# Optimization experiments

Hardware: AMD Instinct MI355X
Metric: run time of the kernel (lower is better)

## Reference

```python
import jax, jax.numpy as jnp
import numpy as np

C_, A_, B_ = 1, 128, 128          # image_size
H, Z, T, N = 512, 128, 16, 32     # h_dim, z_dim, steps, attention grid
EPS = 1e-8
BATCH = 256
PATCH = C_ * N * N                # read/write patch size (C_=1)
IN_ENC = 2 * PATCH + H


def gru_cell(x, h, W_ih, W_hh, b_ih, b_hh):
    gi = x @ W_ih.T + b_ih
    gh = h @ W_hh.T + b_hh
    i_r, i_z, i_n = jnp.split(gi, 3, axis=-1)
    h_r, h_z, h_n = jnp.split(gh, 3, axis=-1)
    r = jax.nn.sigmoid(i_r + h_r)
    z = jax.nn.sigmoid(i_z + h_z)
    n = jnp.tanh(i_n + r * h_n)
    return (1.0 - z) * n + z * h


def filterbank(gt, delta, two_sigma_sq, num_pixels):
    # gt, delta: [b,1]; two_sigma_sq: [b,1,1]
    g = 0.5 * (num_pixels + 1) * (gt + 1.0)                       # [b,1]
    grid = jnp.arange(N, dtype=jnp.float32) - 0.5 * (N - 1)       # [N]
    mu = g + grid[None, :] * delta                                # [b,N]
    pix = jnp.arange(num_pixels, dtype=jnp.float32)               # [P]
    F = jnp.exp(-(pix[None, None, :] - mu[:, :, None]) ** 2 / two_sigma_sq)
    return F / jnp.maximum(F.sum(axis=-1, keepdims=True), EPS)    # [b,N,P]


def get_filterbanks(h_dec, W_attn, b_attn):
    p = h_dec @ W_attn.T + b_attn                                 # [b,5]
    gt_x, gt_y, log_ss, log_dt, log_g = [p[:, i:i + 1] for i in range(5)]
    two_sigma_sq = (2.0 * jnp.exp(log_ss))[:, :, None]            # [b,1,1]
    delta = (max(A_, B_) - 1) * jnp.exp(log_dt) / (N - 1)         # [b,1]
    gamma = jnp.exp(log_g)                                        # [b,1]
    F_x = filterbank(gt_x, delta, two_sigma_sq, A_)               # [b,N,A]
    F_y = filterbank(gt_y, delta, two_sigma_sq, B_)               # [b,N,B]
    return F_x, F_y, gamma


def draw_forward(x, eps, W_ih_enc, W_hh_enc, b_ih_enc, b_hh_enc,
                 W_ih_dec, W_hh_dec, b_ih_dec, b_hh_dec,
                 W_mu, b_mu, W_ls, b_ls, W_wr, b_wr,
                 W_ra, b_ra, W_wa, b_wa):
    b = x.shape[0]
    xf = x.reshape(b, -1)                                         # [b, A*B]
    reconsts0 = jnp.zeros_like(xf)
    h0 = jnp.zeros((b, H), dtype=xf.dtype)

    def step(carry, eps_t):
        reconsts, h_enc, h_dec = carry
        # NOTE: faithful to original: reconsts[-1] is last batch row, broadcast
        x_hat = xf - jax.nn.sigmoid(reconsts[-1])
        # ---- read with attention ----
        F_x, F_y, gamma = get_filterbanks(h_dec, W_ra, b_ra)
        F_x_t = jnp.swapaxes(F_x, -1, -2)                         # [b,A,N]
        img = xf.reshape(b, A_, B_)
        img_hat = x_hat.reshape(b, A_, B_)
        x_attn = (F_y @ img @ F_x_t).reshape(b, -1)               # [b,N*N]
        xh_attn = (F_y @ img_hat @ F_x_t).reshape(b, -1)
        r = gamma * jnp.concatenate([x_attn, xh_attn], axis=1)    # [b,2*N*N]
        # ---- encoder GRU ----
        h_enc = gru_cell(jnp.concatenate([r, h_dec], axis=1), h_enc,
                         W_ih_enc, W_hh_enc, b_ih_enc, b_hh_enc)
        # ---- sample z ~ Q ----
        mu = h_enc @ W_mu.T + b_mu
        sigma = jnp.exp(h_enc @ W_ls.T + b_ls)
        z = mu + eps_t * sigma
        # ---- decoder GRU ----
        h_dec = gru_cell(z, h_dec, W_ih_dec, W_hh_dec, b_ih_dec, b_hh_dec)
        # ---- write with attention ----
        F_xw, F_yw, gamma_w = get_filterbanks(h_dec, W_wa, b_wa)
        w = (h_dec @ W_wr.T + b_wr).reshape(b, N, N)
        wr = (jnp.swapaxes(F_yw, -1, -2) @ w @ F_xw).reshape(b, -1) / gamma_w
        return (reconsts + wr, h_enc, h_dec), None

    (reconsts, _, _), _ = jax.lax.scan(step, (reconsts0, h0, h0), eps)
    return jax.nn.sigmoid(reconsts).reshape(-1, C_, A_, B_)


def setup_inputs() -> dict:
    key = jax.random.key(0)
    ks = jax.random.split(key, 24)
    s = 0.02
    inp = {
        "x": jax.random.uniform(ks[0], (BATCH, C_, A_, B_), jnp.float32),
        "eps": jax.random.normal(ks[1], (T, BATCH, Z), jnp.float32),
        "W_ih_enc": jax.random.normal(ks[2], (3 * H, IN_ENC), jnp.float32) * s,
        "W_hh_enc": jax.random.normal(ks[3], (3 * H, H), jnp.float32) * s,
        "b_ih_enc": jnp.zeros((3 * H,), jnp.float32),
        "b_hh_enc": jnp.zeros((3 * H,), jnp.float32),
        "W_ih_dec": jax.random.normal(ks[4], (3 * H, Z), jnp.float32) * s,
        "W_hh_dec": jax.random.normal(ks[5], (3 * H, H), jnp.float32) * s,
        "b_ih_dec": jnp.zeros((3 * H,), jnp.float32),
        "b_hh_dec": jnp.zeros((3 * H,), jnp.float32),
        "W_mu": jax.random.normal(ks[6], (Z, H), jnp.float32) * s,
        "b_mu": jnp.zeros((Z,), jnp.float32),
        "W_ls": jax.random.normal(ks[7], (Z, H), jnp.float32) * s,
        "b_ls": jnp.zeros((Z,), jnp.float32),
        "W_wr": jax.random.normal(ks[8], (PATCH, H), jnp.float32) * s,
        "b_wr": jnp.zeros((PATCH,), jnp.float32),
        "W_ra": jax.random.normal(ks[9], (5, H), jnp.float32) * s,
        "b_ra": jnp.zeros((5,), jnp.float32),
        "W_wa": jax.random.normal(ks[10], (5, H), jnp.float32) * s,
        "b_wa": jnp.zeros((5,), jnp.float32),
    }
    return inp


def reference(x, eps, W_ih_enc, W_hh_enc, b_ih_enc, b_hh_enc,
              W_ih_dec, W_hh_dec, b_ih_dec, b_hh_dec,
              W_mu, b_mu, W_ls, b_ls, W_wr, b_wr,
              W_ra, b_ra, W_wa, b_wa):
    return draw_forward(x, eps, W_ih_enc, W_hh_enc, b_ih_enc, b_hh_enc,
                        W_ih_dec, W_hh_dec, b_ih_dec, b_hh_dec,
                        W_mu, b_mu, W_ls, b_ls, W_wr, b_wr,
                        W_ra, b_ra, W_wa, b_wa)
```

## Files before the change

### kernel.cpp

```cpp
#include <hip/hip_runtime.h>
#include <math.h>

#define BATCHN 256
#define HDIM 512
#define ZDIM 128
#define NGRID 32
#define ABDIM 128
#define IMGSZ 16384
#define ENCIN 2560
#define G3 1536
#define SPLITK 4

typedef __attribute__((ext_vector_type(8))) short short8;
typedef __attribute__((ext_vector_type(4))) float f32x4;

__device__ __forceinline__ float sigmoidf_(float x){ return 1.0f/(1.0f+expf(-x)); }

__device__ __forceinline__ ushort f2bf_rne(float f){
    union{float f; uint u;} x; x.f=f;
    uint r = (x.u + 0x7FFFu + ((x.u>>16)&1u)) >> 16;
    return (ushort)r;
}
__device__ __forceinline__ float bf2f(ushort h){
    union{uint u; float f;} y; y.u = ((uint)h)<<16;
    return y.f;
}

__global__ void init_slast_k(float* __restrict__ s_last){
    int i = blockIdx.x*256 + threadIdx.x;
    s_last[i] = 0.5f;
}

__global__ void conv_w_k(const float* __restrict__ W, ushort* __restrict__ Wh,
                         ushort* __restrict__ Wl, int n4){
    int i = blockIdx.x*256 + threadIdx.x;
    if(i>=n4) return;
    float4 v = ((const float4*)W)[i];
    float f[4] = {v.x, v.y, v.z, v.w};
    ushort h[4], l[4];
    #pragma unroll
    for(int j=0;j<4;j++){
        h[j] = f2bf_rne(f[j]);
        l[j] = f2bf_rne(f[j] - bf2f(h[j]));
    }
    ushort4 hv; hv.x=h[0]; hv.y=h[1]; hv.z=h[2]; hv.w=h[3];
    ushort4 lv; lv.x=l[0]; lv.y=l[1]; lv.z=l[2]; lv.w=l[3];
    ((ushort4*)Wh)[i] = hv;
    ((ushort4*)Wl)[i] = lv;
}

__device__ __forceinline__ void attn_params_dev512(const float* __restrict__ h,
        const float* __restrict__ W, const float* __restrict__ bvec,
        float* red5 , float* pp , int tid){
    float accp[5];
    #pragma unroll
    for(int i=0;i<5;i++) accp[i]=0.f;
    for(int k=tid;k<HDIM;k+=512){
        float hv = h[k];
        #pragma unroll
        for(int i=0;i<5;i++) accp[i] += hv*W[i*HDIM+k];
    }
    int wv = tid>>6;
    #pragma unroll
    for(int i=0;i<5;i++){
        float a = accp[i];
        #pragma unroll
        for(int o=32;o>0;o>>=1) a += __shfl_down(a,o);
        if((tid&63)==0) red5[i*8+wv]=a;
    }
    __syncthreads();
    if(tid<5){
        float s = bvec[tid];
        #pragma unroll
        for(int w2=0;w2<8;w2++) s += red5[tid*8+w2];
        pp[tid]=s;
    }
    __syncthreads();
}

__device__ __forceinline__ void fill_fb_T(float* fxT, float* fyT, const float* pp, int tid){
    float gx = 64.5f*(pp[0]+1.0f);
    float gy = 64.5f*(pp[1]+1.0f);
    float tss = 2.0f*expf(pp[2]);
    float delta = (127.0f/31.0f)*expf(pp[3]);
    int rr = tid>>3;
    int q  = tid&7;
    int j  = rr&31;
    bool isY = rr>=32;
    float mu = (isY?gy:gx) + ((float)j-15.5f)*delta;
    float v[16]; float s=0.f;
    #pragma unroll
    for(int i=0;i<16;i++){
        float d = (float)(q*16+i)-mu;
        float e = expf(-d*d/tss);
        v[i]=e; s+=e;
    }
    s += __shfl_xor(s,1); s += __shfl_xor(s,2); s += __shfl_xor(s,4);
    float inv = 1.0f/fmaxf(s,1e-8f);
    float* dst = isY? fyT : fxT;
    #pragma unroll
    for(int i=0;i<16;i++) dst[(q*16+i)*32 + j] = v[i]*inv;
    __syncthreads();
}

__device__ __forceinline__ void fill_fb_R(float (*fx)[ABDIM+1], float (*fy)[ABDIM+1], const float* pp, int tid){
    float gx = 64.5f*(pp[0]+1.0f);
    float gy = 64.5f*(pp[1]+1.0f);
    float tss = 2.0f*expf(pp[2]);
    float delta = (127.0f/31.0f)*expf(pp[3]);
    int rr = tid>>3;
    int q  = tid&7;
    int j  = rr&31;
    bool isY = rr>=32;
    float mu = (isY?gy:gx) + ((float)j-15.5f)*delta;
    float v[16]; float s=0.f;
    #pragma unroll
    for(int i=0;i<16;i++){
        float d = (float)(q*16+i)-mu;
        float e = expf(-d*d/tss);
        v[i]=e; s+=e;
    }
    s += __shfl_xor(s,1); s += __shfl_xor(s,2); s += __shfl_xor(s,4);
    float inv = 1.0f/fmaxf(s,1e-8f);
    float* rowp = isY? &fy[j][0] : &fx[j][0];
    #pragma unroll
    for(int i=0;i<16;i++) rowp[q*16+i] = v[i]*inv;
    __syncthreads();
}

__global__ __launch_bounds__(512) void read_attn_k(const float* __restrict__ xf, const float* __restrict__ s_last,
        const float* __restrict__ hdec, const ushort* __restrict__ Hd_h, const ushort* __restrict__ Hd_l,
        const float* __restrict__ W_ra, const float* __restrict__ b_ra,
        ushort* __restrict__ Eh, ushort* __restrict__ El){
    __shared__ float smem[4096 + 8256 + 48];
    float* sFxT = smem;
    float* sFyT = smem + 4096;
    float* tmp  = smem + 4096;
    float* red5 = smem + 4096 + 8256;
    float* pp   = red5 + 40;
    int bb = blockIdx.x; int tid = threadIdx.x;
    const float* h = hdec + bb*HDIM;
    attn_params_dev512(h, W_ra, b_ra, red5, pp, tid);
    float gamma = expf(pp[4]);
    fill_fb_T(sFxT, sFyT, pp, tid);

    const float* img = xf + (size_t)bb*IMGSZ;
    int c = tid & 127;
    int jg = tid >> 7;
    float acc0[8], accS[8];
    #pragma unroll
    for(int i=0;i<8;i++){ acc0[i]=0.f; accS[i]=0.f; }
    for(int k=0;k<ABDIM;k++){
        float s  = img[k*ABDIM + c];
        float sl = s_last[k*ABDIM + c];
        float4 f0 = *(const float4*)&sFyT[k*32 + jg*8];
        float4 f1 = *(const float4*)&sFyT[k*32 + jg*8 + 4];
        acc0[0]+=f0.x*s;  acc0[1]+=f0.y*s;  acc0[2]+=f0.z*s;  acc0[3]+=f0.w*s;
        acc0[4]+=f1.x*s;  acc0[5]+=f1.y*s;  acc0[6]+=f1.z*s;  acc0[7]+=f1.w*s;
        accS[0]+=f0.x*sl; accS[1]+=f0.y*sl; accS[2]+=f0.z*sl; accS[3]+=f0.w*sl;
        accS[4]+=f1.x*sl; accS[5]+=f1.y*sl; accS[6]+=f1.z*sl; accS[7]+=f1.w*sl;
    }
    __syncthreads();
    #pragma unroll
    for(int i=0;i<8;i++){
        int j = jg*8+i;
        tmp[0*32*129 + j*129 + c] = acc0[i];
        tmp[1*32*129 + j*129 + c] = acc0[i] - accS[i];
    }
    __syncthreads();
    {
        int i4 = tid & 7;
        int j  = (tid>>3) & 31;
        int p  = tid >> 8;
        float a0=0.f,a1=0.f,a2=0.f,a3=0.f;
        for(int cc=0; cc<ABDIM; cc++){
            float tv = tmp[p*32*129 + j*129 + cc];
            float4 fx = *(const float4*)&sFxT[cc*32 + i4*4];
            a0 += tv*fx.x; a1 += tv*fx.y; a2 += tv*fx.z; a3 += tv*fx.w;
        }
        float ov[4] = {gamma*a0, gamma*a1, gamma*a2, gamma*a3};
        ushort4 oh, ol;
        ushort hq;
        hq=f2bf_rne(ov[0]); oh.x=hq; ol.x=f2bf_rne(ov[0]-bf2f(hq));
        hq=f2bf_rne(ov[1]); oh.y=hq; ol.y=f2bf_rne(ov[1]-bf2f(hq));
        hq=f2bf_rne(ov[2]); oh.z=hq; ol.z=f2bf_rne(ov[2]-bf2f(hq));
        hq=f2bf_rne(ov[3]); oh.w=hq; ol.w=f2bf_rne(ov[3]-bf2f(hq));
        size_t off = (size_t)bb*ENCIN + p*1024 + j*NGRID + i4*4;
        *(ushort4*)(Eh + off) = oh;
        *(ushort4*)(El + off) = ol;
    }
    {
        int i = tid;
        Eh[(size_t)bb*ENCIN + 2048 + i] = Hd_h[(size_t)bb*HDIM + i];
        El[(size_t)bb*ENCIN + 2048 + i] = Hd_l[(size_t)bb*HDIM + i];
    }
}

__device__ __forceinline__ void gemm_one_bf(const ushort* __restrict__ Ah_g, const ushort* __restrict__ Al_g,
        const ushort* __restrict__ Wh, const ushort* __restrict__ Wl,
        int K, int s, int row0, int col0, int Nn, float* __restrict__ Out,
        ushort* Ah, ushort* Al, ushort* Bh, ushort* Bl, int tid){
    int lane = tid&63, w = tid>>6;
    int m0 = (w>>1)*32, n0 = (w&1)*32;
    int fr = lane&15, kq = (lane>>4)*8;
    int sr = tid>>2, sq = (tid&3)*16;
    int ch = K/SPLITK;
    int kend = (s+1)*ch;
    f32x4 acc[2][2];
    #pragma unroll
    for(int i=0;i<2;i++)
        #pragma unroll
        for(int j=0;j<2;j++) acc[i][j] = (f32x4){0.f,0.f,0.f,0.f};

    for(int k0=s*ch; k0<kend; k0+=64){
        int rem = kend - k0;
        uint4 vah0, vah1, val0, val1, vbh0, vbh1, vbl0, vbl1;
        bool gd = (sq < rem);
        if(gd){
            size_t aoff = (size_t)(row0+sr)*K + k0 + sq;
            size_t boff = (size_t)(col0+sr)*K + k0 + sq;
            vah0 = *(const uint4*)(Ah_g + aoff);
            vah1 = *(const uint4*)(Ah_g + aoff + 8);
            val0 = *(const uint4*)(Al_g + aoff);
            val1 = *(const uint4*)(Al_g + aoff + 8);
            vbh0 = *(const uint4*)(Wh + boff);
            vbh1 = *(const uint4*)(Wh + boff + 8);
            vbl0 = *(const uint4*)(Wl + boff);
            vbl1 = *(const uint4*)(Wl + boff + 8);
        }
        __syncthreads();
        if(gd){
            *(uint4*)&Ah[sr*72 + sq]     = vah0;
            *(uint4*)&Ah[sr*72 + sq + 8] = vah1;
            *(uint4*)&Al[sr*72 + sq]     = val0;
            *(uint4*)&Al[sr*72 + sq + 8] = val1;
            *(uint4*)&Bh[sr*72 + sq]     = vbh0;
            *(uint4*)&Bh[sr*72 + sq + 8] = vbh1;
            *(uint4*)&Bl[sr*72 + sq]     = vbl0;
            *(uint4*)&Bl[sr*72 + sq + 8] = vbl1;
        }
        __syncthreads();
        int nk = (rem>=64)?2:1;
        for(int ks=0; ks<nk; ks++){
            int kb = ks*32 + kq;
            short8 a_h[2], a_l[2], b_h[2], b_l[2];
            #pragma unroll
            for(int mf=0;mf<2;mf++){
                a_h[mf] = *(short8*)&Ah[(m0+mf*16+fr)*72 + kb];
                a_l[mf] = *(short8*)&Al[(m0+mf*16+fr)*72 + kb];
            }
            #pragma unroll
            for(int nf=0;nf<2;nf++){
                b_h[nf] = *(short8*)&Bh[(n0+nf*16+fr)*72 + kb];
                b_l[nf] = *(short8*)&Bl[(n0+nf*16+fr)*72 + kb];
            }
            #pragma unroll
            for(int mf=0;mf<2;mf++)
                #pragma unroll
                for(int nf=0;nf<2;nf++){
                    acc[mf][nf] = __builtin_amdgcn_mfma_f32_16x16x32_bf16(a_h[mf], b_h[nf], acc[mf][nf], 0,0,0);
                    acc[mf][nf] = __builtin_amdgcn_mfma_f32_16x16x32_bf16(a_h[mf], b_l[nf], acc[mf][nf], 0,0,0);
                    acc[mf][nf] = __builtin_amdgcn_mfma_f32_16x16x32_bf16(a_l[mf], b_h[nf], acc[mf][nf], 0,0,0);
                }
        }
    }
    int crow = (lane>>4)*4, ccol = lane&15;
    #pragma unroll
    for(int mf=0;mf<2;mf++)
        #pragma unroll
        for(int nf=0;nf<2;nf++)
            #pragma unroll
            for(int r=0;r<4;r++)
                Out[((size_t)s*BATCHN + row0+m0+mf*16+crow+r)*Nn + col0+n0+nf*16+ccol] = acc[mf][nf][r];
    __syncthreads();
}

__global__ __launch_bounds__(256) void gemm_bf_dual(
        const ushort* __restrict__ A1h, const ushort* __restrict__ A1l,
        const ushort* __restrict__ W1h, const ushort* __restrict__ W1l, int K1,
        const ushort* __restrict__ A2h, const ushort* __restrict__ A2l,
        const ushort* __restrict__ W2h, const ushort* __restrict__ W2l, int K2,
        float* __restrict__ Pi, float* __restrict__ Ph, int Nn){
    __shared__ ushort Ah[64*72], Al[64*72], Bh[64*72], Bl[64*72];
    int tid = threadIdx.x;
    int row0 = blockIdx.y*64, col0 = blockIdx.x*64, s = blockIdx.z;
    gemm_one_bf(A1h, A1l, W1h, W1l, K1, s, row0, col0, Nn, Pi, Ah, Al, Bh, Bl, tid);
    if(K2>0)
        gemm_one_bf(A2h, A2l, W2h, W2l, K2, s, row0, col0, Nn, Ph, Ah, Al, Bh, Bl, tid);
}

__global__ __launch_bounds__(512) void gru_combine_z_k(const float* __restrict__ Pi, const float* __restrict__ Ph,
        const float* __restrict__ bi, const float* __restrict__ bh,
        float* __restrict__ h, ushort* __restrict__ Hh, ushort* __restrict__ Hl,
        const float* __restrict__ Wmu, const float* __restrict__ bmu,
        const float* __restrict__ Wls, const float* __restrict__ bls,
        const float* __restrict__ eps_t, ushort* __restrict__ Zh, ushort* __restrict__ Zl){
    __shared__ float hs[HDIM];
    int bb = blockIdx.x, tid = threadIdx.x;
    int j = tid;
    float gi_r=bi[j], gi_z=bi[512+j], gi_n=bi[1024+j];
    float gh_r=bh[j], gh_z=bh[512+j], gh_n=bh[1024+j];
    #pragma unroll
    for(int s=0;s<SPLITK;s++){
        size_t base = ((size_t)s*BATCHN + bb)*G3 + j;
        gi_r += Pi[base]; gi_z += Pi[base+512]; gi_n += Pi[base+1024];
        gh_r += Ph[base]; gh_z += Ph[base+512]; gh_n += Ph[base+1024];
    }
    float r = sigmoidf_(gi_r + gh_r);
    float z = sigmoidf_(gi_z + gh_z);
    float n = tanhf(gi_n + r*gh_n);
    size_t hoff = (size_t)bb*HDIM + j;
    float hn = (1.f - z)*n + z*h[hoff];
    h[hoff] = hn; hs[j] = hn;
    ushort hh = f2bf_rne(hn);
    Hh[hoff] = hh; Hl[hoff] = f2bf_rne(hn - bf2f(hh));
    __syncthreads();
    int jo = tid>>2, l4 = tid&3;
    float am=0.f, al_=0.f;
    for(int k=l4;k<HDIM;k+=4){
        float hv = hs[k];
        am  += hv*Wmu[(size_t)jo*HDIM+k];
        al_ += hv*Wls[(size_t)jo*HDIM+k];
    }
    am  += __shfl_xor(am,1);  am  += __shfl_xor(am,2);
    al_ += __shfl_xor(al_,1); al_ += __shfl_xor(al_,2);
    if(l4==0){
        float mu = am + bmu[jo];
        float sg = expf(al_ + bls[jo]);
        float zv = mu + eps_t[(size_t)bb*ZDIM + jo]*sg;
        ushort zh = f2bf_rne(zv);
        Zh[(size_t)bb*ZDIM + jo] = zh;
        Zl[(size_t)bb*ZDIM + jo] = f2bf_rne(zv - bf2f(zh));
    }
}

__global__ void gru_combine_bf_k(const float* __restrict__ Pi, const float* __restrict__ Ph,
        const float* __restrict__ bi, const float* __restrict__ bh,
        float* __restrict__ h, ushort* __restrict__ Hh, ushort* __restrict__ Hl){
    int idx = blockIdx.x*256 + threadIdx.x;
    int bb = idx >> 9, j = idx & 511;
    float gi_r=bi[j], gi_z=bi[512+j], gi_n=bi[1024+j];
    float gh_r=bh[j], gh_z=bh[512+j], gh_n=bh[1024+j];
    #pragma unroll
    for(int s=0;s<SPLITK;s++){
        size_t base = ((size_t)s*BATCHN + bb)*G3 + j;
        gi_r += Pi[base]; gi_z += Pi[base+512]; gi_n += Pi[base+1024];
        gh_r += Ph[base]; gh_z += Ph[base+512]; gh_n += Ph[base+1024];
    }
    float r = sigmoidf_(gi_r + gh_r);
    float z = sigmoidf_(gi_z + gh_z);
    float n = tanhf(gi_n + r*gh_n);
    float hn = (1.f - z)*n + z*h[idx];
    h[idx] = hn;
    ushort hh = f2bf_rne(hn);
    Hh[idx] = hh; Hl[idx] = f2bf_rne(hn - bf2f(hh));
}

__global__ __launch_bounds__(512) void write_apply_k(const float* __restrict__ Pw, const float* __restrict__ b_wr,
        const float* __restrict__ hdec, const float* __restrict__ W_wa, const float* __restrict__ b_wa,
        float* __restrict__ rec, float* __restrict__ s_last){
    __shared__ float sFy[NGRID][ABDIM+1];
    __shared__ float sFx[NGRID][ABDIM+1];
    __shared__ float sw[NGRID][36];
    __shared__ float t[ABDIM][36];
    __shared__ float red5[40];
    __shared__ float pp[8];
    int bb = blockIdx.x, tid = threadIdx.x;
    const float* h = hdec + bb*HDIM;
    attn_params_dev512(h, W_wa, b_wa, red5, pp, tid);
    float invg = expf(-pp[4]);
    fill_fb_R(sFx, sFy, pp, tid);
    for(int i=tid;i<NGRID*NGRID;i+=512){
        float a = b_wr[i];
        #pragma unroll
        for(int s=0;s<SPLITK;s++) a += Pw[((size_t)s*BATCHN + bb)*1024 + i];
        sw[i>>5][i&31] = a;
    }
    __syncthreads();
    {
        int p = tid>>2, iq = tid&3;
        float a[8];
        #pragma unroll
        for(int i=0;i<8;i++) a[i]=0.f;
        for(int j=0;j<NGRID;j++){
            float fy = sFy[j][p];
            float4 w0 = *(const float4*)&sw[j][iq*8];
            float4 w1 = *(const float4*)&sw[j][iq*8+4];
            a[0]+=fy*w0.x; a[1]+=fy*w0.y; a[2]+=fy*w0.z; a[3]+=fy*w0.w;
            a[4]+=fy*w1.x; a[5]+=fy*w1.y; a[6]+=fy*w1.z; a[7]+=fy*w1.w;
        }
        float4 o0; o0.x=a[0];o0.y=a[1];o0.z=a[2];o0.w=a[3];
        float4 o1; o1.x=a[4];o1.y=a[5];o1.z=a[6];o1.w=a[7];
        *(float4*)&t[p][iq*8]   = o0;
        *(float4*)&t[p][iq*8+4] = o1;
    }
    __syncthreads();
    {
        int q = tid&127, pg = tid>>7;
        float fxc[32];
        #pragma unroll
        for(int i=0;i<32;i++) fxc[i] = sFx[i][q];
        for(int pi=0; pi<32; pi++){
            int p = pg*32 + pi;
            float acc = 0.f;
            #pragma unroll
            for(int i4=0;i4<8;i4++){
                float4 tv = *(const float4*)&t[p][i4*4];
                acc += tv.x*fxc[i4*4] + tv.y*fxc[i4*4+1] + tv.z*fxc[i4*4+2] + tv.w*fxc[i4*4+3];
            }
            size_t off = (size_t)bb*IMGSZ + p*ABDIM + q;
            float nv = rec[off] + acc*invg;
            rec[off] = nv;
            if(bb==BATCHN-1) s_last[p*ABDIM + q] = sigmoidf_(nv);
        }
    }
}

__global__ void sigmoid_all_k(float* __restrict__ rec){
    int i = blockIdx.x*256 + threadIdx.x;
    rec[i] = sigmoidf_(rec[i]);
}

extern "C" void kernel_launch(void* const* d_in, const int* in_sizes, int n_in,
                              void* d_out, int out_size, void* d_ws, size_t ws_size,
                              hipStream_t stream) {
    const float* x        = (const float*)d_in[0];
    const float* eps      = (const float*)d_in[1];
    const float* W_ih_enc = (const float*)d_in[2];
    const float* W_hh_enc = (const float*)d_in[3];
    const float* b_ih_enc = (const float*)d_in[4];
    const float* b_hh_enc = (const float*)d_in[5];
    const float* W_ih_dec = (const float*)d_in[6];
    const float* W_hh_dec = (const float*)d_in[7];
    const float* b_ih_dec = (const float*)d_in[8];
    const float* b_hh_dec = (const float*)d_in[9];
    const float* W_mu     = (const float*)d_in[10];
    const float* b_mu     = (const float*)d_in[11];
    const float* W_ls     = (const float*)d_in[12];
    const float* b_ls     = (const float*)d_in[13];
    const float* W_wr     = (const float*)d_in[14];
    const float* b_wr     = (const float*)d_in[15];
    const float* W_ra     = (const float*)d_in[16];
    const float* b_ra     = (const float*)d_in[17];
    const float* W_wa     = (const float*)d_in[18];
    const float* b_wa     = (const float*)d_in[19];

    float* rec = (float*)d_out;

    float* ws = (float*)d_ws;
    float* h_enc  = ws;  ws += BATCHN*HDIM;
    float* h_dec  = ws;  ws += BATCHN*HDIM;
    float* s_last = ws;  ws += IMGSZ;
    float* Pi     = ws;  ws += (size_t)SPLITK*BATCHN*G3;
    float* Ph     = ws;  ws += (size_t)SPLITK*BATCHN*G3;
    float* Pw     = Pi;

    ushort* us = (ushort*)ws;
    ushort* Wie_h = us; us += 1536*2560;
    ushort* Wie_l = us; us += 1536*2560;
    ushort* Whe_h = us; us += 1536*512;
    ushort* Whe_l = us; us += 1536*512;
    ushort* Wid_h = us; us += 1536*128;
    ushort* Wid_l = us; us += 1536*128;
    ushort* Whd_h = us; us += 1536*512;
    ushort* Whd_l = us; us += 1536*512;
    ushort* Wwr_h = us; us += 1024*512;
    ushort* Wwr_l = us; us += 1024*512;
    ushort* Eh    = us; us += BATCHN*ENCIN;
    ushort* El    = us; us += BATCHN*ENCIN;
    ushort* He_h  = us; us += BATCHN*HDIM;
    ushort* He_l  = us; us += BATCHN*HDIM;
    ushort* Hd_h  = us; us += BATCHN*HDIM;
    ushort* Hd_l  = us; us += BATCHN*HDIM;
    ushort* Zh    = us; us += BATCHN*ZDIM;
    ushort* Zl    = us; us += BATCHN*ZDIM;

    hipMemsetAsync(rec,   0, (size_t)BATCHN*IMGSZ*sizeof(float), stream);
    hipMemsetAsync(h_enc, 0, (size_t)BATCHN*HDIM*sizeof(float), stream);
    hipMemsetAsync(h_dec, 0, (size_t)BATCHN*HDIM*sizeof(float), stream);
    hipMemsetAsync(He_h,  0, (size_t)BATCHN*HDIM*sizeof(ushort)*2, stream);
    hipMemsetAsync(Hd_h,  0, (size_t)BATCHN*HDIM*sizeof(ushort)*2, stream);
    init_slast_k<<<IMGSZ/256,256,0,stream>>>(s_last);

    conv_w_k<<<(1536*2560/4+255)/256,256,0,stream>>>(W_ih_enc, Wie_h, Wie_l, 1536*2560/4);
    conv_w_k<<<(1536*512/4+255)/256,256,0,stream>>>(W_hh_enc, Whe_h, Whe_l, 1536*512/4);
    conv_w_k<<<(1536*128/4+255)/256,256,0,stream>>>(W_ih_dec, Wid_h, Wid_l, 1536*128/4);
    conv_w_k<<<(1536*512/4+255)/256,256,0,stream>>>(W_hh_dec, Whd_h, Whd_l, 1536*512/4);
    conv_w_k<<<(1024*512/4+255)/256,256,0,stream>>>(W_wr, Wwr_h, Wwr_l, 1024*512/4);

    for(int t=0;t<16;t++){
        read_attn_k<<<BATCHN,512,0,stream>>>(x, s_last, h_dec, Hd_h, Hd_l, W_ra, b_ra, Eh, El);
        gemm_bf_dual<<<dim3(G3/64, BATCHN/64, SPLITK),256,0,stream>>>(
            Eh, El, Wie_h, Wie_l, ENCIN, He_h, He_l, Whe_h, Whe_l, HDIM, Pi, Ph, G3);
        gru_combine_z_k<<<BATCHN,512,0,stream>>>(Pi, Ph, b_ih_enc, b_hh_enc,
            h_enc, He_h, He_l, W_mu, b_mu, W_ls, b_ls, eps + (size_t)t*BATCHN*ZDIM, Zh, Zl);
        gemm_bf_dual<<<dim3(G3/64, BATCHN/64, SPLITK),256,0,stream>>>(
            Zh, Zl, Wid_h, Wid_l, ZDIM, Hd_h, Hd_l, Whd_h, Whd_l, HDIM, Pi, Ph, G3);
        gru_combine_bf_k<<<BATCHN*HDIM/256,256,0,stream>>>(Pi, Ph, b_ih_dec, b_hh_dec, h_dec, Hd_h, Hd_l);
        gemm_bf_dual<<<dim3(1024/64, BATCHN/64, SPLITK),256,0,stream>>>(
            Hd_h, Hd_l, Wwr_h, Wwr_l, HDIM,
            (const ushort*)nullptr, (const ushort*)nullptr, (const ushort*)nullptr, (const ushort*)nullptr, 0,
            Pw, (float*)nullptr, 1024);
        write_apply_k<<<BATCHN,512,0,stream>>>(Pw, b_wr, h_dec, W_wa, b_wa, rec, s_last);
    }
    sigmoid_all_k<<<BATCHN*IMGSZ/256,256,0,stream>>>(rec);
}
```

Measured before the change: 1.694 ms.

## Fuse per-step kernels into one cooperative persistent megakernel with grid syncs

Replaces the roughly 112 per-timestep kernel launches with a single cooperative kernel of 256 blocks that loops over all 16 steps and separates phases with grid-wide barriers. GEMM work is redistributed as explicit jobs with different split-K partitions, and the partial-sum slabs are resized so the hidden-state GEMMs can be computed in other phases. This removes launch overhead and inter-kernel gaps. In exchange it limits parallelism to one 512-thread block per batch row, adds grid-sync cost, and leaves some blocks idle during the smaller GEMM phases.

```diff
diff --git a/kernel.cpp b/kernel.cpp
--- a/kernel.cpp
+++ b/kernel.cpp
@@ -1,5 +1,8 @@
 #include <hip/hip_runtime.h>
+#include <hip/hip_cooperative_groups.h>
 #include <math.h>
+
+namespace cg = cooperative_groups;
 
 #define BATCHN 256
 #define HDIM 512
@@ -9,7 +12,7 @@
 #define IMGSZ 16384
 #define ENCIN 2560
 #define G3 1536
-#define SPLITK 4
+#define SLAB (BATCHN*G3)
 
 typedef __attribute__((ext_vector_type(8))) short short8;
 typedef __attribute__((ext_vector_type(4))) float f32x4;
@@ -49,7 +52,7 @@
     ((ushort4*)Wl)[i] = lv;
 }
 
-__device__ __forceinline__ void attn_params_dev512(const float* __restrict__ h,
+__device__ void attn_params_dev(const float* __restrict__ h,
         const float* __restrict__ W, const float* __restrict__ bvec,
         float* red5 , float* pp , int tid){
     float accp[5];
@@ -78,7 +81,7 @@
     __syncthreads();
 }
 
-__device__ __forceinline__ void fill_fb_T(float* fxT, float* fyT, const float* pp, int tid){
+__device__ void fill_fb_T(float* fxT, float* fyT, const float* pp, int tid){
     float gx = 64.5f*(pp[0]+1.0f);
     float gy = 64.5f*(pp[1]+1.0f);
     float tss = 2.0f*expf(pp[2]);
@@ -103,7 +106,7 @@
     __syncthreads();
 }
 
-__device__ __forceinline__ void fill_fb_R(float (*fx)[ABDIM+1], float (*fy)[ABDIM+1], const float* pp, int tid){
+__device__ void fill_fb_R(float* fx, float* fy, const float* pp, int tid){
     float gx = 64.5f*(pp[0]+1.0f);
     float gy = 64.5f*(pp[1]+1.0f);
     float tss = 2.0f*expf(pp[2]);
@@ -122,137 +125,57 @@
     }
     s += __shfl_xor(s,1); s += __shfl_xor(s,2); s += __shfl_xor(s,4);
     float inv = 1.0f/fmaxf(s,1e-8f);
-    float* rowp = isY? &fy[j][0] : &fx[j][0];
+    float* rowp = (isY? fy : fx) + j*129;
     #pragma unroll
     for(int i=0;i<16;i++) rowp[q*16+i] = v[i]*inv;
     __syncthreads();
 }
 
-__global__ __launch_bounds__(512) void read_attn_k(const float* __restrict__ xf, const float* __restrict__ s_last,
-        const float* __restrict__ hdec, const ushort* __restrict__ Hd_h, const ushort* __restrict__ Hd_l,
-        const float* __restrict__ W_ra, const float* __restrict__ b_ra,
-        ushort* __restrict__ Eh, ushort* __restrict__ El){
-    __shared__ float smem[4096 + 8256 + 48];
-    float* sFxT = smem;
-    float* sFyT = smem + 4096;
-    float* tmp  = smem + 4096;
-    float* red5 = smem + 4096 + 8256;
-    float* pp   = red5 + 40;
-    int bb = blockIdx.x; int tid = threadIdx.x;
-    const float* h = hdec + bb*HDIM;
-    attn_params_dev512(h, W_ra, b_ra, red5, pp, tid);
-    float gamma = expf(pp[4]);
-    fill_fb_T(sFxT, sFyT, pp, tid);
-
-    const float* img = xf + (size_t)bb*IMGSZ;
-    int c = tid & 127;
-    int jg = tid >> 7;
-    float acc0[8], accS[8];
-    #pragma unroll
-    for(int i=0;i<8;i++){ acc0[i]=0.f; accS[i]=0.f; }
-    for(int k=0;k<ABDIM;k++){
-        float s  = img[k*ABDIM + c];
-        float sl = s_last[k*ABDIM + c];
-        float4 f0 = *(const float4*)&sFyT[k*32 + jg*8];
-        float4 f1 = *(const float4*)&sFyT[k*32 + jg*8 + 4];
-        acc0[0]+=f0.x*s;  acc0[1]+=f0.y*s;  acc0[2]+=f0.z*s;  acc0[3]+=f0.w*s;
-        acc0[4]+=f1.x*s;  acc0[5]+=f1.y*s;  acc0[6]+=f1.z*s;  acc0[7]+=f1.w*s;
-        accS[0]+=f0.x*sl; accS[1]+=f0.y*sl; accS[2]+=f0.z*sl; accS[3]+=f0.w*sl;
-        accS[4]+=f1.x*sl; accS[5]+=f1.y*sl; accS[6]+=f1.z*sl; accS[7]+=f1.w*sl;
-    }
-    __syncthreads();
-    #pragma unroll
-    for(int i=0;i<8;i++){
-        int j = jg*8+i;
-        tmp[0*32*129 + j*129 + c] = acc0[i];
-        tmp[1*32*129 + j*129 + c] = acc0[i] - accS[i];
-    }
-    __syncthreads();
-    {
-        int i4 = tid & 7;
-        int j  = (tid>>3) & 31;
-        int p  = tid >> 8;
-        float a0=0.f,a1=0.f,a2=0.f,a3=0.f;
-        for(int cc=0; cc<ABDIM; cc++){
-            float tv = tmp[p*32*129 + j*129 + cc];
-            float4 fx = *(const float4*)&sFxT[cc*32 + i4*4];
-            a0 += tv*fx.x; a1 += tv*fx.y; a2 += tv*fx.z; a3 += tv*fx.w;
-        }
-        float ov[4] = {gamma*a0, gamma*a1, gamma*a2, gamma*a3};
-        ushort4 oh, ol;
-        ushort hq;
-        hq=f2bf_rne(ov[0]); oh.x=hq; ol.x=f2bf_rne(ov[0]-bf2f(hq));
-        hq=f2bf_rne(ov[1]); oh.y=hq; ol.y=f2bf_rne(ov[1]-bf2f(hq));
-        hq=f2bf_rne(ov[2]); oh.z=hq; ol.z=f2bf_rne(ov[2]-bf2f(hq));
-        hq=f2bf_rne(ov[3]); oh.w=hq; ol.w=f2bf_rne(ov[3]-bf2f(hq));
-        size_t off = (size_t)bb*ENCIN + p*1024 + j*NGRID + i4*4;
-        *(ushort4*)(Eh + off) = oh;
-        *(ushort4*)(El + off) = ol;
-    }
-    {
-        int i = tid;
-        Eh[(size_t)bb*ENCIN + 2048 + i] = Hd_h[(size_t)bb*HDIM + i];
-        El[(size_t)bb*ENCIN + 2048 + i] = Hd_l[(size_t)bb*HDIM + i];
-    }
-}
-
-__device__ __forceinline__ void gemm_one_bf(const ushort* __restrict__ Ah_g, const ushort* __restrict__ Al_g,
+__device__ void gemm_job(const ushort* __restrict__ Agh, const ushort* __restrict__ Agl,
         const ushort* __restrict__ Wh, const ushort* __restrict__ Wl,
-        int K, int s, int row0, int col0, int Nn, float* __restrict__ Out,
-        ushort* Ah, ushort* Al, ushort* Bh, ushort* Bl, int tid){
+        int K, int k0, int kiters, int row0, int col0, int Nn, float* __restrict__ Out,
+        ushort* AH, ushort* AL, ushort* BH, ushort* BL, int tid){
     int lane = tid&63, w = tid>>6;
     int m0 = (w>>1)*32, n0 = (w&1)*32;
     int fr = lane&15, kq = (lane>>4)*8;
-    int sr = tid>>2, sq = (tid&3)*16;
-    int ch = K/SPLITK;
-    int kend = (s+1)*ch;
+    int rA = tid>>2, kA = (tid&3)*16;
+    int rB = tid>>3, kB = (tid&7)*8;
     f32x4 acc[2][2];
     #pragma unroll
     for(int i=0;i<2;i++)
         #pragma unroll
-        for(int j=0;j<2;j++) acc[i][j] = (f32x4){0.f,0.f,0.f,0.f};
-
-    for(int k0=s*ch; k0<kend; k0+=64){
-        int rem = kend - k0;
-        uint4 vah0, vah1, val0, val1, vbh0, vbh1, vbl0, vbl1;
-        bool gd = (sq < rem);
-        if(gd){
-            size_t aoff = (size_t)(row0+sr)*K + k0 + sq;
-            size_t boff = (size_t)(col0+sr)*K + k0 + sq;
-            vah0 = *(const uint4*)(Ah_g + aoff);
-            vah1 = *(const uint4*)(Ah_g + aoff + 8);
-            val0 = *(const uint4*)(Al_g + aoff);
-            val1 = *(const uint4*)(Al_g + aoff + 8);
-            vbh0 = *(const uint4*)(Wh + boff);
-            vbh1 = *(const uint4*)(Wh + boff + 8);
-            vbl0 = *(const uint4*)(Wl + boff);
-            vbl1 = *(const uint4*)(Wl + boff + 8);
-        }
+        for(int j=0;j<2;j++) acc[i][j]=(f32x4){0.f,0.f,0.f,0.f};
+    for(int it=0; it<kiters; ++it){
+        int kb = k0 + it*64;
+        size_t aoff = (size_t)(row0+rA)*K + kb + kA;
+        size_t boff = (size_t)(col0+rB)*K + kb + kB;
+        uint4 ah0 = *(const uint4*)(Agh + aoff);
+        uint4 ah1 = *(const uint4*)(Agh + aoff + 8);
+        uint4 al0 = *(const uint4*)(Agl + aoff);
+        uint4 al1 = *(const uint4*)(Agl + aoff + 8);
+        uint4 bh0 = *(const uint4*)(Wh + boff);
+        uint4 bl0 = *(const uint4*)(Wl + boff);
         __syncthreads();
-        if(gd){
-            *(uint4*)&Ah[sr*72 + sq]     = vah0;
-            *(uint4*)&Ah[sr*72 + sq + 8] = vah1;
-            *(uint4*)&Al[sr*72 + sq]     = val0;
-            *(uint4*)&Al[sr*72 + sq + 8] = val1;
-            *(uint4*)&Bh[sr*72 + sq]     = vbh0;
-            *(uint4*)&Bh[sr*72 + sq + 8] = vbh1;
-            *(uint4*)&Bl[sr*72 + sq]     = vbl0;
-            *(uint4*)&Bl[sr*72 + sq + 8] = vbl1;
-        }
+        *(uint4*)&AH[rA*72 + kA]     = ah0;
+        *(uint4*)&AH[rA*72 + kA + 8] = ah1;
+        *(uint4*)&AL[rA*72 + kA]     = al0;
+        *(uint4*)&AL[rA*72 + kA + 8] = al1;
+        *(uint4*)&BH[rB*72 + kB]     = bh0;
+        *(uint4*)&BL[rB*72 + kB]     = bl0;
         __syncthreads();
-        int nk = (rem>=64)?2:1;
-        for(int ks=0; ks<nk; ks++){
-            int kb = ks*32 + kq;
+        #pragma unroll
+        for(int ks=0; ks<2; ks++){
+            int kk = ks*32 + kq;
             short8 a_h[2], a_l[2], b_h[2], b_l[2];
             #pragma unroll
             for(int mf=0;mf<2;mf++){
-                a_h[mf] = *(short8*)&Ah[(m0+mf*16+fr)*72 + kb];
-                a_l[mf] = *(short8*)&Al[(m0+mf*16+fr)*72 + kb];
+                a_h[mf] = *(short8*)&AH[(m0+mf*16+fr)*72 + kk];
+                a_l[mf] = *(short8*)&AL[(m0+mf*16+fr)*72 + kk];
             }
             #pragma unroll
             for(int nf=0;nf<2;nf++){
-                b_h[nf] = *(short8*)&Bh[(n0+nf*16+fr)*72 + kb];
-                b_l[nf] = *(short8*)&Bl[(n0+nf*16+fr)*72 + kb];
+                b_h[nf] = *(short8*)&BH[(n0+nf*16+fr)*72 + kk];
+                b_l[nf] = *(short8*)&BL[(n0+nf*16+fr)*72 + kk];
             }
             #pragma unroll
             for(int mf=0;mf<2;mf++)
@@ -271,154 +194,259 @@
         for(int nf=0;nf<2;nf++)
             #pragma unroll
             for(int r=0;r<4;r++)
-                Out[((size_t)s*BATCHN + row0+m0+mf*16+crow+r)*Nn + col0+n0+nf*16+ccol] = acc[mf][nf][r];
-    __syncthreads();
-}
-
-__global__ __launch_bounds__(256) void gemm_bf_dual(
-        const ushort* __restrict__ A1h, const ushort* __restrict__ A1l,
-        const ushort* __restrict__ W1h, const ushort* __restrict__ W1l, int K1,
-        const ushort* __restrict__ A2h, const ushort* __restrict__ A2l,
-        const ushort* __restrict__ W2h, const ushort* __restrict__ W2l, int K2,
-        float* __restrict__ Pi, float* __restrict__ Ph, int Nn){
-    __shared__ ushort Ah[64*72], Al[64*72], Bh[64*72], Bl[64*72];
+                Out[(size_t)(row0+m0+mf*16+crow+r)*Nn + col0+n0+nf*16+ccol] = acc[mf][nf][r];
+}
+
+struct MegaP {
+    const float *x, *eps;
+    const float *bie, *bhe, *bid_, *bhd;
+    const float *Wmu, *bmu, *Wls, *bls;
+    const float *bwr, *Wra, *bra, *Wwa, *bwa;
+    float *rec, *h_enc, *h_dec, *s_last;
+    const ushort *Wie_h,*Wie_l,*Whe_h,*Whe_l,*Wid_h,*Wid_l,*Whd_h,*Whd_l,*Wwr_h,*Wwr_l;
+    ushort *Eh,*El,*He_h,*He_l,*Hd_h,*Hd_l,*Zh,*Zl;
+    float *Pi,*Ph,*Ph2;
+};
+
+__global__ __launch_bounds__(512) void mega_k(MegaP P){
+    cg::grid_group gg = cg::this_grid();
+    __shared__ __align__(16) char smem_raw[57344];
+    float*  smemF = (float*)smem_raw;
+    ushort* smemU = (ushort*)smem_raw;
+    ushort* AH = smemU;
+    ushort* AL = smemU + 9216;
+    ushort* BH = smemU + 18432;
+    ushort* BL = smemU + 23040;
     int tid = threadIdx.x;
-    int row0 = blockIdx.y*64, col0 = blockIdx.x*64, s = blockIdx.z;
-    gemm_one_bf(A1h, A1l, W1h, W1l, K1, s, row0, col0, Nn, Pi, Ah, Al, Bh, Bl, tid);
-    if(K2>0)
-        gemm_one_bf(A2h, A2l, W2h, W2l, K2, s, row0, col0, Nn, Ph, Ah, Al, Bh, Bl, tid);
-}
-
-__global__ __launch_bounds__(512) void gru_combine_z_k(const float* __restrict__ Pi, const float* __restrict__ Ph,
-        const float* __restrict__ bi, const float* __restrict__ bh,
-        float* __restrict__ h, ushort* __restrict__ Hh, ushort* __restrict__ Hl,
-        const float* __restrict__ Wmu, const float* __restrict__ bmu,
-        const float* __restrict__ Wls, const float* __restrict__ bls,
-        const float* __restrict__ eps_t, ushort* __restrict__ Zh, ushort* __restrict__ Zl){
-    __shared__ float hs[HDIM];
-    int bb = blockIdx.x, tid = threadIdx.x;
-    int j = tid;
-    float gi_r=bi[j], gi_z=bi[512+j], gi_n=bi[1024+j];
-    float gh_r=bh[j], gh_z=bh[512+j], gh_n=bh[1024+j];
-    #pragma unroll
-    for(int s=0;s<SPLITK;s++){
-        size_t base = ((size_t)s*BATCHN + bb)*G3 + j;
-        gi_r += Pi[base]; gi_z += Pi[base+512]; gi_n += Pi[base+1024];
-        gh_r += Ph[base]; gh_z += Ph[base+512]; gh_n += Ph[base+1024];
-    }
-    float r = sigmoidf_(gi_r + gh_r);
-    float z = sigmoidf_(gi_z + gh_z);
-    float n = tanhf(gi_n + r*gh_n);
-    size_t hoff = (size_t)bb*HDIM + j;
-    float hn = (1.f - z)*n + z*h[hoff];
-    h[hoff] = hn; hs[j] = hn;
-    ushort hh = f2bf_rne(hn);
-    Hh[hoff] = hh; Hl[hoff] = f2bf_rne(hn - bf2f(hh));
-    __syncthreads();
-    int jo = tid>>2, l4 = tid&3;
-    float am=0.f, al_=0.f;
-    for(int k=l4;k<HDIM;k+=4){
-        float hv = hs[k];
-        am  += hv*Wmu[(size_t)jo*HDIM+k];
-        al_ += hv*Wls[(size_t)jo*HDIM+k];
-    }
-    am  += __shfl_xor(am,1);  am  += __shfl_xor(am,2);
-    al_ += __shfl_xor(al_,1); al_ += __shfl_xor(al_,2);
-    if(l4==0){
-        float mu = am + bmu[jo];
-        float sg = expf(al_ + bls[jo]);
-        float zv = mu + eps_t[(size_t)bb*ZDIM + jo]*sg;
-        ushort zh = f2bf_rne(zv);
-        Zh[(size_t)bb*ZDIM + jo] = zh;
-        Zl[(size_t)bb*ZDIM + jo] = f2bf_rne(zv - bf2f(zh));
-    }
-}
-
-__global__ void gru_combine_bf_k(const float* __restrict__ Pi, const float* __restrict__ Ph,
-        const float* __restrict__ bi, const float* __restrict__ bh,
-        float* __restrict__ h, ushort* __restrict__ Hh, ushort* __restrict__ Hl){
-    int idx = blockIdx.x*256 + threadIdx.x;
-    int bb = idx >> 9, j = idx & 511;
-    float gi_r=bi[j], gi_z=bi[512+j], gi_n=bi[1024+j];
-    float gh_r=bh[j], gh_z=bh[512+j], gh_n=bh[1024+j];
-    #pragma unroll
-    for(int s=0;s<SPLITK;s++){
-        size_t base = ((size_t)s*BATCHN + bb)*G3 + j;
-        gi_r += Pi[base]; gi_z += Pi[base+512]; gi_n += Pi[base+1024];
-        gh_r += Ph[base]; gh_z += Ph[base+512]; gh_n += Ph[base+1024];
-    }
-    float r = sigmoidf_(gi_r + gh_r);
-    float z = sigmoidf_(gi_z + gh_z);
-    float n = tanhf(gi_n + r*gh_n);
-    float hn = (1.f - z)*n + z*h[idx];
-    h[idx] = hn;
-    ushort hh = f2bf_rne(hn);
-    Hh[idx] = hh; Hl[idx] = f2bf_rne(hn - bf2f(hh));
-}
-
-__global__ __launch_bounds__(512) void write_apply_k(const float* __restrict__ Pw, const float* __restrict__ b_wr,
-        const float* __restrict__ hdec, const float* __restrict__ W_wa, const float* __restrict__ b_wa,
-        float* __restrict__ rec, float* __restrict__ s_last){
-    __shared__ float sFy[NGRID][ABDIM+1];
-    __shared__ float sFx[NGRID][ABDIM+1];
-    __shared__ float sw[NGRID][36];
-    __shared__ float t[ABDIM][36];
-    __shared__ float red5[40];
-    __shared__ float pp[8];
-    int bb = blockIdx.x, tid = threadIdx.x;
-    const float* h = hdec + bb*HDIM;
-    attn_params_dev512(h, W_wa, b_wa, red5, pp, tid);
-    float invg = expf(-pp[4]);
-    fill_fb_R(sFx, sFy, pp, tid);
-    for(int i=tid;i<NGRID*NGRID;i+=512){
-        float a = b_wr[i];
-        #pragma unroll
-        for(int s=0;s<SPLITK;s++) a += Pw[((size_t)s*BATCHN + bb)*1024 + i];
-        sw[i>>5][i&31] = a;
-    }
-    __syncthreads();
-    {
-        int p = tid>>2, iq = tid&3;
-        float a[8];
-        #pragma unroll
-        for(int i=0;i<8;i++) a[i]=0.f;
-        for(int j=0;j<NGRID;j++){
-            float fy = sFy[j][p];
-            float4 w0 = *(const float4*)&sw[j][iq*8];
-            float4 w1 = *(const float4*)&sw[j][iq*8+4];
-            a[0]+=fy*w0.x; a[1]+=fy*w0.y; a[2]+=fy*w0.z; a[3]+=fy*w0.w;
-            a[4]+=fy*w1.x; a[5]+=fy*w1.y; a[6]+=fy*w1.z; a[7]+=fy*w1.w;
-        }
-        float4 o0; o0.x=a[0];o0.y=a[1];o0.z=a[2];o0.w=a[3];
-        float4 o1; o1.x=a[4];o1.y=a[5];o1.z=a[6];o1.w=a[7];
-        *(float4*)&t[p][iq*8]   = o0;
-        *(float4*)&t[p][iq*8+4] = o1;
-    }
-    __syncthreads();
-    {
-        int q = tid&127, pg = tid>>7;
-        float fxc[32];
-        #pragma unroll
-        for(int i=0;i<32;i++) fxc[i] = sFx[i][q];
-        for(int pi=0; pi<32; pi++){
-            int p = pg*32 + pi;
-            float acc = 0.f;
-            #pragma unroll
-            for(int i4=0;i4<8;i4++){
-                float4 tv = *(const float4*)&t[p][i4*4];
-                acc += tv.x*fxc[i4*4] + tv.y*fxc[i4*4+1] + tv.z*fxc[i4*4+2] + tv.w*fxc[i4*4+3];
-            }
-            size_t off = (size_t)bb*IMGSZ + p*ABDIM + q;
-            float nv = rec[off] + acc*invg;
-            rec[off] = nv;
-            if(bb==BATCHN-1) s_last[p*ABDIM + q] = sigmoidf_(nv);
-        }
-    }
-}
-
-__global__ void sigmoid_all_k(float* __restrict__ rec){
-    int i = blockIdx.x*256 + threadIdx.x;
-    rec[i] = sigmoidf_(rec[i]);
+    int blk = blockIdx.x;
+    float* Pw  = P.Pi + SLAB;
+    float* Pi2 = P.Pi;
+
+    for(int t=0; t<16; ++t){
+        const float* eps_t = P.eps + (size_t)t*BATCHN*ZDIM;
+        {
+            float* sFxT = smemF;
+            float* sFyT = smemF + 4096;
+            float* tmp  = smemF + 4096;
+            float* red5 = smemF + 12352;
+            float* pp   = red5 + 40;
+            int bb = blk;
+            const float* h = P.h_dec + (size_t)bb*HDIM;
+            attn_params_dev(h, P.Wra, P.bra, red5, pp, tid);
+            float gamma = expf(pp[4]);
+            fill_fb_T(sFxT, sFyT, pp, tid);
+            const float* img = P.x + (size_t)bb*IMGSZ;
+            int c = tid & 127;
+            int jg = tid >> 7;
+            float acc0[8], accS[8];
+            #pragma unroll
+            for(int i=0;i<8;i++){ acc0[i]=0.f; accS[i]=0.f; }
+            for(int k=0;k<ABDIM;k++){
+                float s  = img[k*ABDIM + c];
+                float sl = P.s_last[k*ABDIM + c];
+                float4 f0 = *(const float4*)&sFyT[k*32 + jg*8];
+                float4 f1 = *(const float4*)&sFyT[k*32 + jg*8 + 4];
+                acc0[0]+=f0.x*s;  acc0[1]+=f0.y*s;  acc0[2]+=f0.z*s;  acc0[3]+=f0.w*s;
+                acc0[4]+=f1.x*s;  acc0[5]+=f1.y*s;  acc0[6]+=f1.z*s;  acc0[7]+=f1.w*s;
+                accS[0]+=f0.x*sl; accS[1]+=f0.y*sl; accS[2]+=f0.z*sl; accS[3]+=f0.w*sl;
+                accS[4]+=f1.x*sl; accS[5]+=f1.y*sl; accS[6]+=f1.z*sl; accS[7]+=f1.w*sl;
+            }
+            __syncthreads();
+            #pragma unroll
+            for(int i=0;i<8;i++){
+                int j = jg*8+i;
+                tmp[0*32*129 + j*129 + c] = acc0[i];
+                tmp[1*32*129 + j*129 + c] = acc0[i] - accS[i];
+            }
+            __syncthreads();
+            {
+                int i4 = tid & 7;
+                int j  = (tid>>3) & 31;
+                int p  = tid >> 8;
+                float a0=0.f,a1=0.f,a2=0.f,a3=0.f;
+                for(int cc=0; cc<ABDIM; cc++){
+                    float tv = tmp[p*32*129 + j*129 + cc];
+                    float4 fx = *(const float4*)&sFxT[cc*32 + i4*4];
+                    a0 += tv*fx.x; a1 += tv*fx.y; a2 += tv*fx.z; a3 += tv*fx.w;
+                }
+                float ov[4] = {gamma*a0, gamma*a1, gamma*a2, gamma*a3};
+                ushort4 oh, ol; ushort hq;
+                hq=f2bf_rne(ov[0]); oh.x=hq; ol.x=f2bf_rne(ov[0]-bf2f(hq));
+                hq=f2bf_rne(ov[1]); oh.y=hq; ol.y=f2bf_rne(ov[1]-bf2f(hq));
+                hq=f2bf_rne(ov[2]); oh.z=hq; ol.z=f2bf_rne(ov[2]-bf2f(hq));
+                hq=f2bf_rne(ov[3]); oh.w=hq; ol.w=f2bf_rne(ov[3]-bf2f(hq));
+                size_t off = (size_t)bb*ENCIN + p*1024 + j*NGRID + i4*4;
+                *(ushort4*)(P.Eh + off) = oh;
+                *(ushort4*)(P.El + off) = ol;
+            }
+            P.Eh[(size_t)bb*ENCIN + 2048 + tid] = P.Hd_h[(size_t)bb*HDIM + tid];
+            P.El[(size_t)bb*ENCIN + 2048 + tid] = P.Hd_l[(size_t)bb*HDIM + tid];
+        }
+        gg.sync();
+        for(int job=blk; job<432; job+=256){
+            const ushort *Ah_,*Al_,*Wh_,*Wl_; int K_,k0_,ki_,r0_,c0_; float* Out_;
+            if(job < 240){
+                int tt2 = job % 48, s = job / 48;
+                Ah_=P.Eh; Al_=P.El; Wh_=P.Wie_h; Wl_=P.Wie_l;
+                K_=ENCIN; k0_=s*512; ki_=8;
+                r0_=(tt2/24)*128; c0_=(tt2%24)*64;
+                Out_ = P.Pi + (size_t)s*SLAB;
+            } else if(job < 336){
+                int jj = job-240; int tt2 = jj % 48, s = jj / 48;
+                Ah_=P.He_h; Al_=P.He_l; Wh_=P.Whe_h; Wl_=P.Whe_l;
+                K_=HDIM; k0_=s*256; ki_=4;
+                r0_=(tt2/24)*128; c0_=(tt2%24)*64;
+                Out_ = P.Ph + (size_t)s*SLAB;
+            } else {
+                int jj = job-336; int tt2 = jj % 48, s = jj / 48;
+                Ah_=P.Hd_h; Al_=P.Hd_l; Wh_=P.Whd_h; Wl_=P.Whd_l;
+                K_=HDIM; k0_=s*256; ki_=4;
+                r0_=(tt2/24)*128; c0_=(tt2%24)*64;
+                Out_ = P.Ph2 + (size_t)s*SLAB;
+            }
+            gemm_job(Ah_, Al_, Wh_, Wl_, K_, k0_, ki_, r0_, c0_, G3, Out_, AH, AL, BH, BL, tid);
+        }
+        gg.sync();
+        {
+            float* hs = smemF;
+            int bb = blk, j = tid;
+            float gi_r=P.bie[j], gi_z=P.bie[512+j], gi_n=P.bie[1024+j];
+            float gh_r=P.bhe[j], gh_z=P.bhe[512+j], gh_n=P.bhe[1024+j];
+            #pragma unroll
+            for(int s=0;s<5;s++){
+                size_t base = (size_t)s*SLAB + (size_t)bb*G3 + j;
+                gi_r += P.Pi[base]; gi_z += P.Pi[base+512]; gi_n += P.Pi[base+1024];
+            }
+            #pragma unroll
+            for(int s=0;s<2;s++){
+                size_t base = (size_t)s*SLAB + (size_t)bb*G3 + j;
+                gh_r += P.Ph[base]; gh_z += P.Ph[base+512]; gh_n += P.Ph[base+1024];
+            }
+            float r = sigmoidf_(gi_r + gh_r);
+            float z = sigmoidf_(gi_z + gh_z);
+            float n = tanhf(gi_n + r*gh_n);
+            size_t hoff = (size_t)bb*HDIM + j;
+            float hn = (1.f - z)*n + z*P.h_enc[hoff];
+            P.h_enc[hoff] = hn; hs[j] = hn;
+            ushort hh = f2bf_rne(hn);
+            P.He_h[hoff] = hh; P.He_l[hoff] = f2bf_rne(hn - bf2f(hh));
+            __syncthreads();
+            int jo = tid>>2, l4 = tid&3;
+            float am=0.f, al_=0.f;
+            for(int k=l4;k<HDIM;k+=4){
+                float hv = hs[k];
+                am  += hv*P.Wmu[(size_t)jo*HDIM+k];
+                al_ += hv*P.Wls[(size_t)jo*HDIM+k];
+            }
+            am  += __shfl_xor(am,1);  am  += __shfl_xor(am,2);
+            al_ += __shfl_xor(al_,1); al_ += __shfl_xor(al_,2);
+            if(l4==0){
+                float mu = am + P.bmu[jo];
+                float sg = expf(al_ + P.bls[jo]);
+                float zv = mu + eps_t[(size_t)bb*ZDIM + jo]*sg;
+                ushort zh = f2bf_rne(zv);
+                P.Zh[(size_t)bb*ZDIM + jo] = zh;
+                P.Zl[(size_t)bb*ZDIM + jo] = f2bf_rne(zv - bf2f(zh));
+            }
+        }
+        gg.sync();
+        if(blk < 48){
+            int tt2 = blk;
+            gemm_job(P.Zh, P.Zl, P.Wid_h, P.Wid_l, ZDIM, 0, 2,
+                     (tt2/24)*128, (tt2%24)*64, G3, Pi2, AH, AL, BH, BL, tid);
+        }
+        gg.sync();
+        {
+            int idx = blk*512 + tid;
+            int bb = idx>>9, j = idx&511;
+            float gi_r=P.bid_[j], gi_z=P.bid_[512+j], gi_n=P.bid_[1024+j];
+            float gh_r=P.bhd[j], gh_z=P.bhd[512+j], gh_n=P.bhd[1024+j];
+            {
+                size_t base = (size_t)bb*G3 + j;
+                gi_r += Pi2[base]; gi_z += Pi2[base+512]; gi_n += Pi2[base+1024];
+            }
+            #pragma unroll
+            for(int s=0;s<2;s++){
+                size_t base = (size_t)s*SLAB + (size_t)bb*G3 + j;
+                gh_r += P.Ph2[base]; gh_z += P.Ph2[base+512]; gh_n += P.Ph2[base+1024];
+            }
+            float r = sigmoidf_(gi_r + gh_r);
+            float z = sigmoidf_(gi_z + gh_z);
+            float n = tanhf(gi_n + r*gh_n);
+            float hn = (1.f - z)*n + z*P.h_dec[idx];
+            P.h_dec[idx] = hn;
+            ushort hh = f2bf_rne(hn);
+            P.Hd_h[idx] = hh; P.Hd_l[idx] = f2bf_rne(hn - bf2f(hh));
+        }
+        gg.sync();
+        if(blk < 128){
+            int tt2 = blk % 32, s = blk / 32;
+            gemm_job(P.Hd_h, P.Hd_l, P.Wwr_h, P.Wwr_l, HDIM, s*128, 2,
+                     (tt2/16)*128, (tt2%16)*64, 1024, Pw + (size_t)s*BATCHN*1024,
+                     AH, AL, BH, BL, tid);
+        }
+        gg.sync();
+        {
+            float* sFy  = smemF;
+            float* sFx  = smemF + 4128;
+            float* sw   = smemF + 8256;
+            float* tt2  = smemF + 9408;
+            float* red5 = smemF + 14016;
+            float* pp   = red5 + 40;
+            int bb = blk;
+            const float* h = P.h_dec + (size_t)bb*HDIM;
+            attn_params_dev(h, P.Wwa, P.bwa, red5, pp, tid);
+            float invg = expf(-pp[4]);
+            fill_fb_R(sFx, sFy, pp, tid);
+            for(int i=tid;i<NGRID*NGRID;i+=512){
+                float a = P.bwr[i];
+                #pragma unroll
+                for(int s=0;s<4;s++) a += Pw[(size_t)s*BATCHN*1024 + (size_t)bb*1024 + i];
+                sw[(i>>5)*36 + (i&31)] = a;
+            }
+            __syncthreads();
+            {
+                int p = tid>>2, iq = tid&3;
+                float a[8];
+                #pragma unroll
+                for(int i=0;i<8;i++) a[i]=0.f;
+                for(int j=0;j<NGRID;j++){
+                    float fy = sFy[j*129 + p];
+                    float4 w0 = *(const float4*)&sw[j*36 + iq*8];
+                    float4 w1 = *(const float4*)&sw[j*36 + iq*8 + 4];
+                    a[0]+=fy*w0.x; a[1]+=fy*w0.y; a[2]+=fy*w0.z; a[3]+=fy*w0.w;
+                    a[4]+=fy*w1.x; a[5]+=fy*w1.y; a[6]+=fy*w1.z; a[7]+=fy*w1.w;
+                }
+                float4 o0; o0.x=a[0];o0.y=a[1];o0.z=a[2];o0.w=a[3];
+                float4 o1; o1.x=a[4];o1.y=a[5];o1.z=a[6];o1.w=a[7];
+                *(float4*)&tt2[p*36 + iq*8]     = o0;
+                *(float4*)&tt2[p*36 + iq*8 + 4] = o1;
+            }
+            __syncthreads();
+            {
+                int q = tid&127, pg = tid>>7;
+                float fxc[32];
+                #pragma unroll
+                for(int i=0;i<32;i++) fxc[i] = sFx[i*129 + q];
+                for(int pi=0; pi<32; pi++){
+                    int p = pg*32 + pi;
+                    float acc = 0.f;
+                    #pragma unroll
+                    for(int i4=0;i4<8;i4++){
+                        float4 tv = *(const float4*)&tt2[p*36 + i4*4];
+                        acc += tv.x*fxc[i4*4] + tv.y*fxc[i4*4+1] + tv.z*fxc[i4*4+2] + tv.w*fxc[i4*4+3];
+                    }
+                    size_t off = (size_t)bb*IMGSZ + p*ABDIM + q;
+                    float nv = P.rec[off] + acc*invg;
+                    P.rec[off] = nv;
+                    if(bb==BATCHN-1) P.s_last[p*ABDIM + q] = sigmoidf_(nv);
+                }
+            }
+        }
+        gg.sync();
+    }
+    for(size_t i = (size_t)blk*512 + tid; i < (size_t)BATCHN*IMGSZ; i += 131072)
+        P.rec[i] = sigmoidf_(P.rec[i]);
 }
 
 extern "C" void kernel_launch(void* const* d_in, const int* in_sizes, int n_in,
@@ -451,9 +479,9 @@
     float* h_enc  = ws;  ws += BATCHN*HDIM;
     float* h_dec  = ws;  ws += BATCHN*HDIM;
     float* s_last = ws;  ws += IMGSZ;
-    float* Pi     = ws;  ws += (size_t)SPLITK*BATCHN*G3;
-    float* Ph     = ws;  ws += (size_t)SPLITK*BATCHN*G3;
-    float* Pw     = Pi;
+    float* Pi     = ws;  ws += (size_t)5*SLAB;
+    float* Ph     = ws;  ws += (size_t)2*SLAB;
+    float* Ph2    = ws;  ws += (size_t)2*SLAB;
 
     ushort* us = (ushort*)ws;
     ushort* Wie_h = us; us += 1536*2560;
@@ -488,20 +516,19 @@
     conv_w_k<<<(1536*512/4+255)/256,256,0,stream>>>(W_hh_dec, Whd_h, Whd_l, 1536*512/4);
     conv_w_k<<<(1024*512/4+255)/256,256,0,stream>>>(W_wr, Wwr_h, Wwr_l, 1024*512/4);
 
-    for(int t=0;t<16;t++){
-        read_attn_k<<<BATCHN,512,0,stream>>>(x, s_last, h_dec, Hd_h, Hd_l, W_ra, b_ra, Eh, El);
-        gemm_bf_dual<<<dim3(G3/64, BATCHN/64, SPLITK),256,0,stream>>>(
-            Eh, El, Wie_h, Wie_l, ENCIN, He_h, He_l, Whe_h, Whe_l, HDIM, Pi, Ph, G3);
-        gru_combine_z_k<<<BATCHN,512,0,stream>>>(Pi, Ph, b_ih_enc, b_hh_enc,
-            h_enc, He_h, He_l, W_mu, b_mu, W_ls, b_ls, eps + (size_t)t*BATCHN*ZDIM, Zh, Zl);
-        gemm_bf_dual<<<dim3(G3/64, BATCHN/64, SPLITK),256,0,stream>>>(
-            Zh, Zl, Wid_h, Wid_l, ZDIM, Hd_h, Hd_l, Whd_h, Whd_l, HDIM, Pi, Ph, G3);
-        gru_combine_bf_k<<<BATCHN*HDIM/256,256,0,stream>>>(Pi, Ph, b_ih_dec, b_hh_dec, h_dec, Hd_h, Hd_l);
-        gemm_bf_dual<<<dim3(1024/64, BATCHN/64, SPLITK),256,0,stream>>>(
-            Hd_h, Hd_l, Wwr_h, Wwr_l, HDIM,
-            (const ushort*)nullptr, (const ushort*)nullptr, (const ushort*)nullptr, (const ushort*)nullptr, 0,
-            Pw, (float*)nullptr, 1024);
-        write_apply_k<<<BATCHN,512,0,stream>>>(Pw, b_wr, h_dec, W_wa, b_wa, rec, s_last);
-    }
-    sigmoid_all_k<<<BATCHN*IMGSZ/256,256,0,stream>>>(rec);
-}
+    MegaP mp;
+    mp.x = x; mp.eps = eps;
+    mp.bie = b_ih_enc; mp.bhe = b_hh_enc; mp.bid_ = b_ih_dec; mp.bhd = b_hh_dec;
+    mp.Wmu = W_mu; mp.bmu = b_mu; mp.Wls = W_ls; mp.bls = b_ls;
+    mp.bwr = b_wr; mp.Wra = W_ra; mp.bra = b_ra; mp.Wwa = W_wa; mp.bwa = b_wa;
+    mp.rec = rec; mp.h_enc = h_enc; mp.h_dec = h_dec; mp.s_last = s_last;
+    mp.Wie_h=Wie_h; mp.Wie_l=Wie_l; mp.Whe_h=Whe_h; mp.Whe_l=Whe_l;
+    mp.Wid_h=Wid_h; mp.Wid_l=Wid_l; mp.Whd_h=Whd_h; mp.Whd_l=Whd_l;
+    mp.Wwr_h=Wwr_h; mp.Wwr_l=Wwr_l;
+    mp.Eh=Eh; mp.El=El; mp.He_h=He_h; mp.He_l=He_l; mp.Hd_h=Hd_h; mp.Hd_l=Hd_l;
+    mp.Zh=Zh; mp.Zl=Zl;
+    mp.Pi=Pi; mp.Ph=Ph; mp.Ph2=Ph2;
+
+    void* kargs[] = { (void*)&mp };
+    hipLaunchCooperativeKernel(mega_k, dim3(256), dim3(512), kargs, 0u, stream);
+}
```

New measurement: 5.277 ms. 211% more time.
